# Kernel optimization log

Measured on AMD Instinct MI355X. Metric: run time of the kernel, lower is better.

The kernel has to match this reference:

```python
import jax, jax.numpy as jnp
import numpy as np


def setup_inputs() -> dict:
    key = jax.random.key(0)
    k1, k2 = jax.random.split(key)
    N, C, H, W = 8, 3, 512, 1024
    img = jax.random.normal(k1, (N, C, H, W), dtype=jnp.float32)
    flo = jax.random.normal(k2, (N, 2, H, W), dtype=jnp.float32)
    return {"img": img, "flo": flo}


def _splat(img_nhwc, ix, iy, w, H, W):
    # img_nhwc: (N,H,W,C); ix,iy: int32 (N,H,W) absolute target coords; w: (N,H,W)
    N = img_nhwc.shape[0]
    C = img_nhwc.shape[-1]
    valid = (ix >= 0) & (ix < H) & (iy >= 0) & (iy < W)
    w = jnp.where(valid, w, 0.0)
    ixc = jnp.clip(ix, 0, H - 1)
    iyc = jnp.clip(iy, 0, W - 1)
    n_idx = jnp.arange(N, dtype=jnp.int32)[:, None, None]
    tid = (n_idx * H + ixc) * W + iyc            # (N,H,W) flat index into N*H*W
    tid = tid.reshape(-1)
    vals = (img_nhwc * w[..., None]).reshape(-1, C)
    imgw = jnp.zeros((N * H * W, C), dtype=img_nhwc.dtype).at[tid].add(vals)
    onew = jnp.zeros((N * H * W,), dtype=img_nhwc.dtype).at[tid].add(w.reshape(-1))
    imgw = imgw.reshape(N, H, W, C).transpose(0, 3, 1, 2)          # (N,C,H,W)
    onew = jnp.broadcast_to(onew.reshape(N, 1, H, W), (N, C, H, W))
    return imgw, onew


def _forward(img, flo):
    N, C, H, W = img.shape
    y = flo[:, 0]                                # (N,H,W) row offset
    x = flo[:, 1]                                # (N,H,W) col offset
    x1 = jnp.floor(x); x2 = x1 + 1.0
    y1 = jnp.floor(y); y2 = y1 + 1.0
    # gaussian splat weights
    dx1 = (x - x1) ** 2; dx2 = (x - x2) ** 2
    dy1 = (y - y1) ** 2; dy2 = (y - y2) ** 2
    w11 = jnp.exp(-(dx1 + dy1)); w12 = jnp.exp(-(dx1 + dy2))
    w21 = jnp.exp(-(dx2 + dy1)); w22 = jnp.exp(-(dx2 + dy2))
    # base grid + integer shift -> absolute target coords
    bx = jnp.arange(H, dtype=jnp.int32)[None, :, None]   # row index
    by = jnp.arange(W, dtype=jnp.int32)[None, None, :]   # col index
    img_nhwc = img.transpose(0, 2, 3, 1)
    out = []
    for sx, sy, w in ((x1, y1, w11), (x1, y2, w12), (x2, y1, w21), (x2, y2, w22)):
        ix = sx.astype(jnp.int32) + bx
        iy = sy.astype(jnp.int32) + by
        out.append(_splat(img_nhwc, ix, iy, w, H, W))
    imgw = out[0][0] + out[1][0] + out[2][0] + out[3][0]
    o = out[0][1] + out[1][1] + out[2][1] + out[3][1]
    return imgw, o


def reference(img, flo):
    return _forward(img, flo)
```

## Files before the change

kernel.cpp:

```cpp
#include <hip/hip_runtime.h>
#include <hip/hip_fp16.h>
#include <stdint.h>

constexpr int Nn = 8;
constexpr int Cc = 3;
constexpr int Hh = 512;
constexpr int Ww = 1024;
constexpr int HW = Hh * Ww;
constexpr int NCHW = Nn * Cc * HW;

constexpr int TH = 16;
constexpr int TW = 32;
constexpr int R  = 4;
constexpr int RH = TH + 2 * R;
constexpr int RW = TW + 2 * R;
constexpr int NPIX = RH * RW;
constexpr int ITERS = (NPIX + 255) / 256;
constexpr int TILE_PIX = TH * TW;
constexpr int AWP = TW + 1;
constexpr int NP  = (TH + 1) * AWP;
constexpr int NSLOT = 3;
constexpr int OVF_CAP = 128;

typedef float fvec4 __attribute__((ext_vector_type(4)));
typedef float fvec2 __attribute__((ext_vector_type(2)));

__global__ __launch_bounds__(256, 6) void splat_tiled(
        const float* __restrict__ img,
        const float* __restrict__ flo,
        float* __restrict__ out) {
    __shared__ unsigned int s_tag[NP];
    __shared__ unsigned int s_pay[NSLOT * NP * 3];
    __shared__ unsigned int s_kcnt[(NP + 3) / 4 + 1];
    __shared__ unsigned int s_ovf[OVF_CAP * 4];
    __shared__ unsigned int s_ovfn;
    const int tid = threadIdx.x;
    for (int i = tid; i < NP; i += 256) s_tag[i] = 0u;
    for (int i = tid; i < (NP + 3) / 4 + 1; i += 256) s_kcnt[i] = 0u;
    if (tid == 0) s_ovfn = 0u;
    __syncthreads();

    const int lin = blockIdx.x + 32 * blockIdx.y + 1024 * blockIdx.z;
    const int n   = lin & 7;
    const int t   = lin >> 3;
    const int tw0 = (t & 31) * TW;
    const int th0 = (t >> 5) * TH;
    const float* __restrict__ floy = flo + (size_t)(n * 2 + 0) * HW;
    const float* __restrict__ flox = flo + (size_t)(n * 2 + 1) * HW;
    const float* __restrict__ imgn = img + (size_t)n * Cc * HW;

    float sy[ITERS], sx[ITERS], u0[ITERS], u1[ITERS], u2[ITERS];
    #pragma unroll
    for (int it = 0; it < ITERS; ++it) {
        int i  = tid + 256 * it;
        int ic = i < NPIX ? i : NPIX - 1;
        int rh = ic / RW;
        int rw = ic - rh * RW;
        int h  = th0 - R + rh;
        int w  = tw0 - R + rw;
        int hc = h < 0 ? 0 : (h > Hh - 1 ? Hh - 1 : h);
        int wc = w < 0 ? 0 : (w > Ww - 1 ? Ww - 1 : w);
        int hwc = hc * Ww + wc;
        sy[it] = floy[hwc];
        sx[it] = flox[hwc];
        u0[it] = imgn[hwc];
        u1[it] = imgn[HW + hwc];
        u2[it] = imgn[2 * HW + hwc];
    }

    int aA[ITERS];
    unsigned int tg[ITERS], q0[ITERS], q1[ITERS], q2[ITERS];
    bool pend[ITERS];
    #pragma unroll
    for (int it = 0; it < ITERS; ++it) {
        int i  = tid + 256 * it;
        int rh = i / RW;
        int rw = i - rh * RW;
        int h  = th0 - R + rh;
        int w  = tw0 - R + rw;
        bool live = (i < NPIX) & (h >= 0) & (h < Hh) & (w >= 0) & (w < Ww);

        float y = sy[it], x = sx[it];
        float x1f = floorf(x), y1f = floorf(y);
        float fx = x - x1f, fy = y - y1f;
        int ox = (int)x1f, oy = (int)y1f;
        bool patchok = (ox >= -R) & (ox <= R - 1) & (oy >= -R) & (oy <= R - 1);
        int ah = ox + rh - R;
        int aw = oy + rw - R;
        bool rec = live & patchok & (ah >= -1) & (ah <= TH - 1)
                                  & (aw >= -1) & (aw <= TW - 1);
        int aIdx = (ah + 1) * AWP + (aw + 1);
        tg[it] = 0x80000000u | ((unsigned)(ox + R) << 3) | (unsigned)(oy + R);
        unsigned h0 = __half_as_ushort(__float2half_rn(u0[it]));
        unsigned h1 = __half_as_ushort(__float2half_rn(u1[it]));
        unsigned h2 = __half_as_ushort(__float2half_rn(u2[it]));
        unsigned fxq = (unsigned)(fx * 65535.0f + 0.5f);
        unsigned fyq = (unsigned)(fy * 65535.0f + 0.5f);
        q0[it] = h0 | (h1 << 16);
        q1[it] = h2 | (fxq << 16);
        q2[it] = fyq | (((unsigned)(ah + 1) & 0x3Fu) << 16)
                     | (((unsigned)(aw + 1) & 0x3Fu) << 22);
        aA[it]  = aIdx;
        pend[it] = rec;
        if (rec) s_tag[aIdx] = tg[it];
    }
    __syncthreads();

    #pragma unroll
    for (int r = 0; r < NSLOT; ++r) {
        #pragma unroll
        for (int it = 0; it < ITERS; ++it) {
            if (pend[it] && s_tag[aA[it]] == tg[it]) {
                int base = aA[it] * 9 + r * 3;
                s_pay[base]     = q0[it];
                s_pay[base + 1] = q1[it];
                s_pay[base + 2] = q2[it];
                ((unsigned char*)s_kcnt)[aA[it]] = (unsigned char)(r + 1);
                pend[it] = false;
            } else if (r == NSLOT - 1 && pend[it]) {
                unsigned idx = atomicAdd(&s_ovfn, 1u);
                if (idx < (unsigned)OVF_CAP) {
                    int b4 = (int)idx * 4;
                    s_ovf[b4]     = q0[it];
                    s_ovf[b4 + 1] = q1[it];
                    s_ovf[b4 + 2] = q2[it];
                }
            }
        }
        __syncthreads();
        if (r < NSLOT - 1) {
            #pragma unroll
            for (int it = 0; it < ITERS; ++it)
                if (pend[it]) s_tag[aA[it]] = tg[it];
            __syncthreads();
        }
    }

    float* __restrict__ imgw  = out;
    float* __restrict__ o_out = out + NCHW;
    const size_t nb = (size_t)n * Cc * HW;
    {
        int pix = 2 * tid;
        int lh = pix >> 5, lw = pix & 31;
        float s0a = 0.f, s0b = 0.f;
        float s1a = 0.f, s1b = 0.f;
        float s2a = 0.f, s2b = 0.f;
        float s3a = 0.f, s3b = 0.f;

        auto apply_entry = [&](unsigned w0, unsigned w1, unsigned w2, int a, int c) {
            float h0 = __half2float(__ushort_as_half((unsigned short)(w0 & 0xFFFFu)));
            float h1 = __half2float(__ushort_as_half((unsigned short)(w0 >> 16)));
            float h2 = __half2float(__ushort_as_half((unsigned short)(w1 & 0xFFFFu)));
            float fx = (float)(w1 >> 16) * (1.0f / 65535.0f);
            float fy = (float)(w2 & 0xFFFFu) * (1.0f / 65535.0f);
            float dx  = fx - (float)a;
            float dxx = dx * dx;
            if (c < 2) {
                float dy = fy - (float)(1 - c);
                float wt = __expf(-(dxx + dy * dy));
                s0a += h0 * wt; s1a += h1 * wt; s2a += h2 * wt; s3a += wt;
            }
            if (c >= 1) {
                float dy = fy - (float)(2 - c);
                float wt = __expf(-(dxx + dy * dy));
                s0b += h0 * wt; s1b += h1 * wt; s2b += h2 * wt; s3b += wt;
            }
        };

        #pragma unroll
        for (int a = 0; a < 2; ++a) {
            int arow = (lh - a + 1) * AWP + lw;
            #pragma unroll
            for (int c = 0; c < 3; ++c) {
                int ai = arow + c;
                int k = ((const unsigned char*)s_kcnt)[ai];
                #pragma unroll
                for (int j = 0; j < NSLOT; ++j) {
                    if (j < k) {
                        int base = ai * 9 + j * 3;
                        apply_entry(s_pay[base], s_pay[base + 1], s_pay[base + 2], a, c);
                    }
                }
            }
        }

        unsigned novf = s_ovfn;
        if (novf > (unsigned)OVF_CAP) novf = OVF_CAP;
        for (unsigned e = 0; e < novf; ++e) {
            unsigned w0 = s_ovf[e * 4];
            unsigned w1 = s_ovf[e * 4 + 1];
            unsigned w2 = s_ovf[e * 4 + 2];
            int ar = (int)((w2 >> 16) & 0x3Fu);
            int ac = (int)((w2 >> 22) & 0x3Fu);
            int a  = lh + 1 - ar;
            int c  = ac - lw;
            if (((unsigned)a < 2u) & ((unsigned)c < 3u))
                apply_entry(w0, w1, w2, a, c);
        }

        size_t hw = (size_t)(th0 + lh) * Ww + (tw0 + lw);
        fvec2 v;
        v[0] = s0a; v[1] = s0b;
        __builtin_nontemporal_store(v, (fvec2*)(imgw + nb + hw));
        v[0] = s1a; v[1] = s1b;
        __builtin_nontemporal_store(v, (fvec2*)(imgw + nb + HW + hw));
        v[0] = s2a; v[1] = s2b;
        __builtin_nontemporal_store(v, (fvec2*)(imgw + nb + 2 * HW + hw));
        v[0] = s3a; v[1] = s3b;
        __builtin_nontemporal_store(v, (fvec2*)(o_out + nb + hw));
        __builtin_nontemporal_store(v, (fvec2*)(o_out + nb + HW + hw));
        __builtin_nontemporal_store(v, (fvec2*)(o_out + nb + 2 * HW + hw));
    }
}

__global__ __launch_bounds__(256) void rescan_all(
        const float* __restrict__ img,
        const float* __restrict__ flo,
        float* __restrict__ out) {
    float* imgw  = out;
    float* o_out = out + NCHW;
    unsigned int j = blockIdx.x * blockDim.x + threadIdx.x;
    if (j >= (unsigned)(Nn * HW / 4)) return;
    int n   = j / (HW / 4);
    int q   = j - n * (HW / 4);
    int hw0 = q * 4;
    const fvec4 y4 = *(const fvec4*)&flo[(size_t)(n * 2 + 0) * HW + hw0];
    const fvec4 x4 = *(const fvec4*)&flo[(size_t)(n * 2 + 1) * HW + hw0];
    #pragma unroll
    for (int k = 0; k < 4; ++k) {
        float x = x4[k], y = y4[k];
        if (x >= -(float)R && x < (float)R && y >= -(float)R && y < (float)R) continue;
        int hw = hw0 + k;
        int h = hw >> 10;
        int w = hw & (Ww - 1);
        float x1f = floorf(x), y1f = floorf(y);
        float fx = x - x1f, fy = y - y1f;
        int bx = (int)x1f, by = (int)y1f;
        float i0 = img[(size_t)(n * Cc + 0) * HW + hw];
        float i1 = img[(size_t)(n * Cc + 1) * HW + hw];
        float i2 = img[(size_t)(n * Cc + 2) * HW + hw];
        const size_t nb = (size_t)n * Cc * HW;
        #pragma unroll
        for (int a = 0; a < 2; ++a) {
            #pragma unroll
            for (int b = 0; b < 2; ++b) {
                int ix = h + bx + a;
                int iy = w + by + b;
                if (ix < 0 || ix >= Hh || iy < 0 || iy >= Ww) continue;
                float dx = fx - (float)a, dy = fy - (float)b;
                float wt = __expf(-(dx * dx + dy * dy));
                int t = ix * Ww + iy;
                atomicAdd(&imgw[nb + t], i0 * wt);
                atomicAdd(&imgw[nb + HW + t], i1 * wt);
                atomicAdd(&imgw[nb + 2 * HW + t], i2 * wt);
                atomicAdd(&o_out[nb + t], wt);
                atomicAdd(&o_out[nb + HW + t], wt);
                atomicAdd(&o_out[nb + 2 * HW + t], wt);
            }
        }
    }
}

extern "C" void kernel_launch(void* const* d_in, const int* in_sizes, int n_in,
                              void* d_out, int out_size, void* d_ws, size_t ws_size,
                              hipStream_t stream) {
    const float* img = (const float*)d_in[0];
    const float* flo = (const float*)d_in[1];
    float* out = (float*)d_out;
    (void)d_ws; (void)ws_size;

    dim3 block(256);
    dim3 grid(32, 32, 8);
    splat_tiled<<<grid, block, 0, stream>>>(img, flo, out);
    rescan_all<<<(Nn * HW / 4 + 255) / 256, 256, 0, stream>>>(img, flo, out);
}
```

Baseline: 191.9 us.

## Precompute factored gaussian splat weights at producer and pack 16-byte LDS entries

```diff
diff --git a/kernel.cpp b/kernel.cpp
--- a/kernel.cpp
+++ b/kernel.cpp
@@ -16,7 +16,6 @@
 constexpr int RW = TW + 2 * R;
 constexpr int NPIX = RH * RW;
 constexpr int ITERS = (NPIX + 255) / 256;
-constexpr int TILE_PIX = TH * TW;
 constexpr int AWP = TW + 1;
 constexpr int NP  = (TH + 1) * AWP;
 constexpr int NSLOT = 3;
@@ -24,15 +23,16 @@
 
 typedef float fvec4 __attribute__((ext_vector_type(4)));
 typedef float fvec2 __attribute__((ext_vector_type(2)));
-
-__global__ __launch_bounds__(256, 6) void splat_tiled(
+typedef unsigned int uvec4 __attribute__((ext_vector_type(4)));
+
+__global__ __launch_bounds__(256, 5) void splat_tiled(
         const float* __restrict__ img,
         const float* __restrict__ flo,
         float* __restrict__ out) {
     __shared__ unsigned int s_tag[NP];
-    __shared__ unsigned int s_pay[NSLOT * NP * 3];
+    __shared__ alignas(16) unsigned int s_pay[NSLOT * NP * 4];
     __shared__ unsigned int s_kcnt[(NP + 3) / 4 + 1];
-    __shared__ unsigned int s_ovf[OVF_CAP * 4];
+    __shared__ alignas(16) unsigned int s_ovf[OVF_CAP * 4];
     __shared__ unsigned int s_ovfn;
     const int tid = threadIdx.x;
     for (int i = tid; i < NP; i += 256) s_tag[i] = 0u;
@@ -69,7 +69,7 @@
     }
 
     int aA[ITERS];
-    unsigned int tg[ITERS], q0[ITERS], q1[ITERS], q2[ITERS];
+    unsigned int tg[ITERS], q0[ITERS], q1[ITERS], q2[ITERS], q3[ITERS];
     bool pend[ITERS];
     #pragma unroll
     for (int it = 0; it < ITERS; ++it) {
@@ -91,15 +91,24 @@
                                   & (aw >= -1) & (aw <= TW - 1);
         int aIdx = (ah + 1) * AWP + (aw + 1);
         tg[it] = 0x80000000u | ((unsigned)(ox + R) << 3) | (unsigned)(oy + R);
+
+        float W00 = __expf(-(fx * fx + fy * fy));
+        float Exf = __expf(2.0f * fx - 1.0f);
+        float Eyf = __expf(2.0f * fy - 1.0f);
+        float W10 = W00 * Exf;
+        float W01 = W00 * Eyf;
+        float W11 = W10 * Eyf;
+
         unsigned h0 = __half_as_ushort(__float2half_rn(u0[it]));
         unsigned h1 = __half_as_ushort(__float2half_rn(u1[it]));
         unsigned h2 = __half_as_ushort(__float2half_rn(u2[it]));
-        unsigned fxq = (unsigned)(fx * 65535.0f + 0.5f);
-        unsigned fyq = (unsigned)(fy * 65535.0f + 0.5f);
+        unsigned meta = ((unsigned)(ah + 1) & 0x3Fu) | (((unsigned)(aw + 1) & 0x3Fu) << 6);
         q0[it] = h0 | (h1 << 16);
-        q1[it] = h2 | (fxq << 16);
-        q2[it] = fyq | (((unsigned)(ah + 1) & 0x3Fu) << 16)
-                     | (((unsigned)(aw + 1) & 0x3Fu) << 22);
+        q1[it] = h2 | (meta << 16);
+        q2[it] = (unsigned)(W00 * 65535.0f + 0.5f)
+               | ((unsigned)(W10 * 65535.0f + 0.5f) << 16);
+        q3[it] = (unsigned)(W01 * 65535.0f + 0.5f)
+               | ((unsigned)(W11 * 65535.0f + 0.5f) << 16);
         aA[it]  = aIdx;
         pend[it] = rec;
         if (rec) s_tag[aIdx] = tg[it];
@@ -111,19 +120,15 @@
         #pragma unroll
         for (int it = 0; it < ITERS; ++it) {
             if (pend[it] && s_tag[aA[it]] == tg[it]) {
-                int base = aA[it] * 9 + r * 3;
-                s_pay[base]     = q0[it];
-                s_pay[base + 1] = q1[it];
-                s_pay[base + 2] = q2[it];
+                uvec4 e = {q0[it], q1[it], q2[it], q3[it]};
+                *(uvec4*)&s_pay[(aA[it] * NSLOT + r) * 4] = e;
                 ((unsigned char*)s_kcnt)[aA[it]] = (unsigned char)(r + 1);
                 pend[it] = false;
             } else if (r == NSLOT - 1 && pend[it]) {
                 unsigned idx = atomicAdd(&s_ovfn, 1u);
                 if (idx < (unsigned)OVF_CAP) {
-                    int b4 = (int)idx * 4;
-                    s_ovf[b4]     = q0[it];
-                    s_ovf[b4 + 1] = q1[it];
-                    s_ovf[b4 + 2] = q2[it];
+                    uvec4 e = {q0[it], q1[it], q2[it], q3[it]};
+                    *(uvec4*)&s_ovf[(int)idx * 4] = e;
                 }
             }
         }
@@ -142,30 +147,8 @@
     {
         int pix = 2 * tid;
         int lh = pix >> 5, lw = pix & 31;
-        float s0a = 0.f, s0b = 0.f;
-        float s1a = 0.f, s1b = 0.f;
-        float s2a = 0.f, s2b = 0.f;
-        float s3a = 0.f, s3b = 0.f;
-
-        auto apply_entry = [&](unsigned w0, unsigned w1, unsigned w2, int a, int c) {
-            float h0 = __half2float(__ushort_as_half((unsigned short)(w0 & 0xFFFFu)));
-            float h1 = __half2float(__ushort_as_half((unsigned short)(w0 >> 16)));
-            float h2 = __half2float(__ushort_as_half((unsigned short)(w1 & 0xFFFFu)));
-            float fx = (float)(w1 >> 16) * (1.0f / 65535.0f);
-            float fy = (float)(w2 & 0xFFFFu) * (1.0f / 65535.0f);
-            float dx  = fx - (float)a;
-            float dxx = dx * dx;
-            if (c < 2) {
-                float dy = fy - (float)(1 - c);
-                float wt = __expf(-(dxx + dy * dy));
-                s0a += h0 * wt; s1a += h1 * wt; s2a += h2 * wt; s3a += wt;
-            }
-            if (c >= 1) {
-                float dy = fy - (float)(2 - c);
-                float wt = __expf(-(dxx + dy * dy));
-                s0b += h0 * wt; s1b += h1 * wt; s2b += h2 * wt; s3b += wt;
-            }
-        };
+        fvec2 a0 = {0.f, 0.f}, a1 = {0.f, 0.f}, a2 = {0.f, 0.f}, a3 = {0.f, 0.f};
+        const uvec4* pay4 = (const uvec4*)s_pay;
 
         #pragma unroll
         for (int a = 0; a < 2; ++a) {
@@ -177,8 +160,26 @@
                 #pragma unroll
                 for (int j = 0; j < NSLOT; ++j) {
                     if (j < k) {
-                        int base = ai * 9 + j * 3;
-                        apply_entry(s_pay[base], s_pay[base + 1], s_pay[base + 2], a, c);
+                        uvec4 e = pay4[ai * NSLOT + j];
+                        float h0 = __half2float(__ushort_as_half((unsigned short)(e.x & 0xFFFFu)));
+                        float h1 = __half2float(__ushort_as_half((unsigned short)(e.x >> 16)));
+                        float h2 = __half2float(__ushort_as_half((unsigned short)(e.y & 0xFFFFu)));
+                        if (c == 0) {
+                            unsigned uw = (e.w >> (16 * a)) & 0xFFFFu;
+                            float wt = (float)uw * (1.0f / 65535.0f);
+                            a0.x += h0 * wt; a1.x += h1 * wt; a2.x += h2 * wt; a3.x += wt;
+                        } else if (c == 1) {
+                            unsigned u0w = (e.z >> (16 * a)) & 0xFFFFu;
+                            unsigned u1w = (e.w >> (16 * a)) & 0xFFFFu;
+                            fvec2 wt = {(float)u0w * (1.0f / 65535.0f),
+                                        (float)u1w * (1.0f / 65535.0f)};
+                            fvec2 v0 = {h0, h0}, v1 = {h1, h1}, v2 = {h2, h2};
+                            a0 += v0 * wt; a1 += v1 * wt; a2 += v2 * wt; a3 += wt;
+                        } else {
+                            unsigned uw = (e.z >> (16 * a)) & 0xFFFFu;
+                            float wt = (float)uw * (1.0f / 65535.0f);
+                            a0.y += h0 * wt; a1.y += h1 * wt; a2.y += h2 * wt; a3.y += wt;
+                        }
                     }
                 }
             }
@@ -186,30 +187,35 @@
 
         unsigned novf = s_ovfn;
         if (novf > (unsigned)OVF_CAP) novf = OVF_CAP;
-        for (unsigned e = 0; e < novf; ++e) {
-            unsigned w0 = s_ovf[e * 4];
-            unsigned w1 = s_ovf[e * 4 + 1];
-            unsigned w2 = s_ovf[e * 4 + 2];
-            int ar = (int)((w2 >> 16) & 0x3Fu);
-            int ac = (int)((w2 >> 22) & 0x3Fu);
+        for (unsigned ei = 0; ei < novf; ++ei) {
+            uvec4 e = ((const uvec4*)s_ovf)[ei];
+            unsigned meta = e.y >> 16;
+            int ar = (int)(meta & 0x3Fu);
+            int ac = (int)((meta >> 6) & 0x3Fu);
             int a  = lh + 1 - ar;
             int c  = ac - lw;
-            if (((unsigned)a < 2u) & ((unsigned)c < 3u))
-                apply_entry(w0, w1, w2, a, c);
+            if (((unsigned)a < 2u) & ((unsigned)c < 3u)) {
+                float h0 = __half2float(__ushort_as_half((unsigned short)(e.x & 0xFFFFu)));
+                float h1 = __half2float(__ushort_as_half((unsigned short)(e.x >> 16)));
+                float h2 = __half2float(__ushort_as_half((unsigned short)(e.y & 0xFFFFu)));
+                unsigned sh = (unsigned)a * 16u;
+                float wb0 = (float)((e.z >> sh) & 0xFFFFu) * (1.0f / 65535.0f);
+                float wb1 = (float)((e.w >> sh) & 0xFFFFu) * (1.0f / 65535.0f);
+                float wt0 = (c == 0) ? wb1 : ((c == 1) ? wb0 : 0.f);
+                float wt1 = (c == 2) ? wb0 : ((c == 1) ? wb1 : 0.f);
+                fvec2 wt = {wt0, wt1};
+                fvec2 v0 = {h0, h0}, v1 = {h1, h1}, v2 = {h2, h2};
+                a0 += v0 * wt; a1 += v1 * wt; a2 += v2 * wt; a3 += wt;
+            }
         }
 
         size_t hw = (size_t)(th0 + lh) * Ww + (tw0 + lw);
-        fvec2 v;
-        v[0] = s0a; v[1] = s0b;
-        __builtin_nontemporal_store(v, (fvec2*)(imgw + nb + hw));
-        v[0] = s1a; v[1] = s1b;
-        __builtin_nontemporal_store(v, (fvec2*)(imgw + nb + HW + hw));
-        v[0] = s2a; v[1] = s2b;
-        __builtin_nontemporal_store(v, (fvec2*)(imgw + nb + 2 * HW + hw));
-        v[0] = s3a; v[1] = s3b;
-        __builtin_nontemporal_store(v, (fvec2*)(o_out + nb + hw));
-        __builtin_nontemporal_store(v, (fvec2*)(o_out + nb + HW + hw));
-        __builtin_nontemporal_store(v, (fvec2*)(o_out + nb + 2 * HW + hw));
+        __builtin_nontemporal_store(a0, (fvec2*)(imgw + nb + hw));
+        __builtin_nontemporal_store(a1, (fvec2*)(imgw + nb + HW + hw));
+        __builtin_nontemporal_store(a2, (fvec2*)(imgw + nb + 2 * HW + hw));
+        __builtin_nontemporal_store(a3, (fvec2*)(o_out + nb + hw));
+        __builtin_nontemporal_store(a3, (fvec2*)(o_out + nb + HW + hw));
+        __builtin_nontemporal_store(a3, (fvec2*)(o_out + nb + 2 * HW + hw));
     }
 }
 
```

Result: no change. 194.8 us (+1.5%).
